# Kernel optimization log

Measured on AMD Instinct MI355X. Metric: run time of the kernel, lower is better.

The kernel has to match this reference:

```python
import jax, jax.numpy as jnp
import numpy as np

EPS = 1e-5

def _bn(x, gamma, beta, mean, var):
    # channel axis = 1; inference-style batchnorm with given stats
    shape = (1, -1) + (1,) * (x.ndim - 2)
    inv = gamma / jnp.sqrt(var + EPS)
    return x * inv.reshape(shape) + (beta - mean * inv).reshape(shape)

def _gather(f, idx):
    # f: (C, N), idx: (N, ns) -> (C, N, ns)
    return f[:, idx]

def setup_inputs() -> dict:
    key = jax.random.key(0)
    ks = jax.random.split(key, 24)
    B, N, C, NS, O = 4, 32768, 64, 16, 128
    inp = {}
    inp['xyz'] = jax.random.normal(ks[0], (B, N, 3), jnp.float32)
    inp['feature'] = jax.random.normal(ks[1], (B, C, N), jnp.float32)
    inp['idx'] = jax.random.randint(ks[2], (B, N, NS), 0, N, jnp.int64 if jax.config.jax_enable_x64 else jnp.int32)
    inp['W1'] = jax.random.normal(ks[3], (64, 3), jnp.float32)
    inp['b1'] = jax.random.normal(ks[4], (64,), jnp.float32)
    inp['g1'] = jax.random.uniform(ks[5], (64,), jnp.float32)
    inp['be1'] = jax.random.normal(ks[6], (64,), jnp.float32)
    inp['m1'] = jnp.zeros((64,), jnp.float32)
    inp['v1'] = jnp.ones((64,), jnp.float32)
    inp['W2'] = jax.random.normal(ks[7], (64, 64), jnp.float32)
    inp['b2'] = jax.random.normal(ks[8], (64,), jnp.float32)
    inp['g2'] = jax.random.uniform(ks[9], (64,), jnp.float32)
    inp['be2'] = jax.random.normal(ks[10], (64,), jnp.float32)
    inp['m2'] = jnp.zeros((64,), jnp.float32)
    inp['v2'] = jnp.ones((64,), jnp.float32)
    inp['W3'] = jax.random.normal(ks[11], (64, 64), jnp.float32)
    inp['b3'] = jax.random.normal(ks[12], (64,), jnp.float32)
    inp['Wf'] = jax.random.normal(ks[13], (O, C * 64), jnp.float32)
    inp['bf'] = jax.random.normal(ks[14], (O,), jnp.float32)
    inp['gf'] = jax.random.uniform(ks[15], (O,), jnp.float32)
    inp['bef'] = jax.random.normal(ks[16], (O,), jnp.float32)
    inp['mf'] = jnp.zeros((O,), jnp.float32)
    inp['vf'] = jnp.ones((O,), jnp.float32)
    return inp

def reference(xyz, feature, idx, W1, b1, g1, be1, m1, v1, W2, b2, g2, be2, m2, v2, W3, b3, Wf, bf, gf, bef, mf, vf):
    B, C, N = feature.shape
    xyz_t = jnp.transpose(xyz, (0, 2, 1))  # (B, 3, N)
    # grouped relative positions: (B, 3, N, ns)
    grouped_xyz = jax.vmap(_gather)(xyz_t, idx) - xyz_t[:, :, :, None]
    # WeightNet: Conv2d 1x1 layers on channel dim
    h = jnp.einsum('oc,bcns->bons', W1, grouped_xyz) + b1[None, :, None, None]
    h = jax.nn.relu(_bn(h, g1, be1, m1, v1))
    h = jnp.einsum('oc,bcns->bons', W2, h) + b2[None, :, None, None]
    h = jax.nn.relu(_bn(h, g2, be2, m2, v2))
    weights = jnp.einsum('oc,bcns->bons', W3, h) + b3[None, :, None, None]  # (B, 64, N, ns)
    # gather features per neighbor: (B, C, N, ns)
    gfeat = jax.vmap(_gather)(feature, idx)
    # per-point matmul (B,N,C,ns) @ (B,N,ns,64) -> (B,N,C,64) -> (B,N,C*64)
    agg = jnp.einsum('bcns,bwns->bncw', gfeat, weights).reshape(B, N, C * weights.shape[1])
    # final Conv1d 1x1 + BN + ReLU, output (B, O, N)
    y = jnp.einsum('of,bnf->bon', Wf, agg) + bf[None, :, None]
    return jax.nn.relu(_bn(y, gf, bef, mf, vf))
```

## Files before the change

### kernel.cpp

```cpp
#include <hip/hip_runtime.h>
#include <cstdint>
#include <cstddef>

#define EPSV 1e-5f
constexpr int Bn  = 4;
constexpr int Nn  = 32768;
constexpr int Cn  = 64;
constexpr int NSn = 16;
constexpr int On  = 128;
constexpr int Pn  = 32;
constexpr int MAIN_BLOCKS = Bn * (Nn / Pn);

typedef __attribute__((ext_vector_type(8))) short short8;
typedef __attribute__((ext_vector_type(4))) float f32x4;

static __device__ __forceinline__ unsigned short f2bf(float f) {
  union { float f; unsigned u; } v; v.f = f;
  unsigned r = v.u + 0x7fffu + ((v.u >> 16) & 1u);
  return (unsigned short)(r >> 16);
}
static __device__ __forceinline__ unsigned pack2(unsigned short a, unsigned short b) {
  return (unsigned)a | ((unsigned)b << 16);
}

constexpr size_t WS_FEATT = 0;
constexpr size_t WS_WFP   = 16u * 1024 * 1024;
constexpr size_t WS_PF    = 17u * 1024 * 1024;
constexpr size_t WS_W2F   = WS_PF + 4096;
constexpr size_t WS_W3B   = WS_W2F + 8192;

__global__ void k_params(const float* __restrict__ W1, const float* __restrict__ b1,
                         const float* __restrict__ g1, const float* __restrict__ be1,
                         const float* __restrict__ m1, const float* __restrict__ v1,
                         const float* __restrict__ W2, const float* __restrict__ b2,
                         const float* __restrict__ g2, const float* __restrict__ be2,
                         const float* __restrict__ m2, const float* __restrict__ v2,
                         const float* __restrict__ W3, const float* __restrict__ b3,
                         const float* __restrict__ bf_, const float* __restrict__ gf,
                         const float* __restrict__ bef, const float* __restrict__ mf,
                         const float* __restrict__ vf,
                         float* __restrict__ pf, unsigned short* __restrict__ W2f,
                         unsigned short* __restrict__ W3b) {
  int t = threadIdx.x;
  if (t < 64) {
    float inv1 = g1[t] * rsqrtf(v1[t] + EPSV);
    pf[t * 4 + 0] = W1[t * 3 + 0] * inv1;
    pf[t * 4 + 1] = W1[t * 3 + 1] * inv1;
    pf[t * 4 + 2] = W1[t * 3 + 2] * inv1;
    pf[t * 4 + 3] = 0.f;
    pf[256 + t] = b1[t] * inv1 + be1[t] - m1[t] * inv1;
    float inv2 = g2[t] * rsqrtf(v2[t] + EPSV);
    pf[320 + t] = b2[t] * inv2 + be2[t] - m2[t] * inv2;
    pf[384 + t] = b3[t];
    for (int k = 0; k < 64; ++k) {
      W2f[t * 64 + k] = f2bf(W2[t * 64 + k] * inv2);
      W3b[t * 64 + k] = f2bf(W3[t * 64 + k]);
    }
  }
  if (t < 128) {
    float invf = gf[t] * rsqrtf(vf[t] + EPSV);
    pf[448 + t] = bf_[t] * invf + bef[t] - mf[t] * invf;
  }
}

__global__ void k_featT(const float* __restrict__ feat, unsigned short* __restrict__ featT) {
  int blk = blockIdx.x;
  int b = blk >> 9;
  int n0 = (blk & 511) << 6;
  __shared__ float tile[64][65];
  int t = threadIdx.x;
  int n_in = t & 63;
  int c4 = t >> 6;
  const float* fb = feat + (size_t)b * Cn * Nn;
#pragma unroll
  for (int k = 0; k < 16; ++k) {
    int c = c4 * 16 + k;
    tile[c][n_in] = fb[(size_t)c * Nn + n0 + n_in];
  }
  __syncthreads();
  unsigned short* outp = featT + ((size_t)b * Nn + n0) * Cn;
  int cc = t & 63;
#pragma unroll
  for (int k = 0; k < 16; ++k) {
    int nn = c4 * 16 + k;
    outp[(size_t)nn * Cn + cc] = f2bf(tile[cc][nn]);
  }
}

__global__ void k_wfp(const float* __restrict__ Wf, const float* __restrict__ gf,
                      const float* __restrict__ vf, unsigned short* __restrict__ WfP) {
  int e = blockIdx.x * 256 + threadIdx.x;
  int rec = e >> 9, wi_ = e & 511;
  int l = wi_ >> 3, j = wi_ & 7;
  int q = rec >> 6, ks = (rec >> 3) & 7, ot = rec & 7;
  int o = ot * 16 + (l & 15);
  int kk = ks * 32 + (l >> 4) * 8 + j;
  int c = (q >> 2) * 16 + (kk >> 4);
  int w = (q & 3) * 16 + (kk & 15);
  float invf = gf[o] * rsqrtf(vf[o] + EPSV);
  WfP[e] = f2bf(Wf[(size_t)o * 4096 + c * 64 + w] * invf);
}

constexpr int SMEM_MAIN = 141312;

__launch_bounds__(512, 1)
__global__ void k_main(const float* __restrict__ xyz, const int* __restrict__ idx,
                       const unsigned short* __restrict__ featT,
                       const unsigned short* __restrict__ WfP,
                       const float* __restrict__ pf,
                       const unsigned short* __restrict__ W2f,
                       const unsigned short* __restrict__ W3b,
                       float* __restrict__ outp) {
  extern __shared__ __align__(16) char smem[];
  unsigned short* wbuf   = (unsigned short*)(smem);
  unsigned short* h1     = (unsigned short*)(smem + 65536);
  unsigned short* gbuf   = (unsigned short*)(smem + 65536);
  unsigned short* h2     = (unsigned short*)(smem + 98304);
  unsigned short* aggbuf = (unsigned short*)(smem + 98304);
  float4* gxbuf = (float4*)(smem + 131072);
  int*    idxbuf = (int*)(smem + 139264);

  const int t = threadIdx.x;
  const int lane = t & 63;
  const int wv = t >> 6;
  const int lq = lane >> 4;
  const int lm = lane & 15;
  const int blk = blockIdx.x;
  const int bb = blk >> 10;
  const int n0 = (blk & 1023) * Pn;

  const float* W1f = pf;
  const float* b1f = pf + 256;
  const float* b2f = pf + 320;
  const float* b3f = pf + 384;
  const float* bff = pf + 448;

  const short8 z8 = {0, 0, 0, 0, 0, 0, 0, 0};
  const f32x4  z4 = {0.f, 0.f, 0.f, 0.f};

  if (t < 256) {
    const float* xb = xyz + (size_t)bb * Nn * 3;
#pragma unroll
    for (int a = 0; a < 2; ++a) {
      int col = t + a * 256;
      int p_ = col >> 4, s_ = col & 15;
      int iv = idx[((size_t)bb * Nn + n0 + p_) * NSn + s_];
      idxbuf[col] = iv;
      float cx = xb[(size_t)(n0 + p_) * 3 + 0];
      float cy = xb[(size_t)(n0 + p_) * 3 + 1];
      float cz = xb[(size_t)(n0 + p_) * 3 + 2];
      gxbuf[col] = make_float4(xb[(size_t)iv * 3 + 0] - cx,
                               xb[(size_t)iv * 3 + 1] - cy,
                               xb[(size_t)iv * 3 + 2] - cz, 0.f);
    }
  }
  __syncthreads();

  for (int h = 0; h < 2; ++h) {
    if (wv < 4) {
#pragma unroll
      for (int a = 0; a < 8; ++a) {
        int aid = t + a * 256;
        int col = aid & 255;
        int oct = aid >> 8;
        float4 g = gxbuf[h * 256 + col];
        unsigned short vals[8];
#pragma unroll
        for (int jj = 0; jj < 8; ++jj) {
          int ch = oct * 8 + jj;
          float v = W1f[ch * 4 + 0] * g.x + W1f[ch * 4 + 1] * g.y +
                    W1f[ch * 4 + 2] * g.z + b1f[ch];
          vals[jj] = f2bf(fmaxf(v, 0.f));
        }
        int u = oct ^ (col & 7);
        uint4 wv4;
        wv4.x = pack2(vals[0], vals[1]); wv4.y = pack2(vals[2], vals[3]);
        wv4.z = pack2(vals[4], vals[5]); wv4.w = pack2(vals[6], vals[7]);
        *(uint4*)(h1 + (size_t)col * 64 + u * 8) = wv4;
      }
    }
    __syncthreads();

    if (wv < 4) {
      f32x4 acc2[4][4];
#pragma unroll
      for (int mt = 0; mt < 4; ++mt)
#pragma unroll
        for (int nt = 0; nt < 4; ++nt) acc2[mt][nt] = z4;
      short8 afr[4][2];
#pragma unroll
      for (int mt = 0; mt < 4; ++mt)
#pragma unroll
        for (int ks = 0; ks < 2; ++ks)
          afr[mt][ks] = *(const short8*)(W2f + (mt * 16 + lm) * 64 + ks * 32 + lq * 8);
#pragma unroll
      for (int nt = 0; nt < 4; ++nt) {
        int col = wv * 64 + nt * 16 + lm;
#pragma unroll
        for (int ks = 0; ks < 2; ++ks) {
          int u = (ks * 4 + lq) ^ (col & 7);
          short8 bfr = *(short8*)(h1 + (size_t)col * 64 + u * 8);
#pragma unroll
          for (int mt = 0; mt < 4; ++mt)
            acc2[mt][nt] = __builtin_amdgcn_mfma_f32_16x16x32_bf16(afr[mt][ks], bfr, acc2[mt][nt], 0, 0, 0);
        }
      }
#pragma unroll
      for (int mt = 0; mt < 4; ++mt)
#pragma unroll
        for (int nt = 0; nt < 4; ++nt) {
          int col = wv * 64 + nt * 16 + lm;
#pragma unroll
          for (int r = 0; r < 4; ++r) {
            int ch = mt * 16 + lq * 4 + r;
            float v = fmaxf(acc2[mt][nt][r] + b2f[ch], 0.f);
            int u = (ch >> 3) ^ (col & 7);
            h2[(size_t)col * 64 + u * 8 + (ch & 7)] = f2bf(v);
          }
        }
    }
    __syncthreads();

    if (wv < 4) {
      f32x4 acc3[4][4];
#pragma unroll
      for (int mt = 0; mt < 4; ++mt)
#pragma unroll
        for (int nt = 0; nt < 4; ++nt) acc3[mt][nt] = z4;
      short8 afr[4][2];
#pragma unroll
      for (int mt = 0; mt < 4; ++mt)
#pragma unroll
        for (int ks = 0; ks < 2; ++ks)
          afr[mt][ks] = *(const short8*)(W3b + (mt * 16 + lm) * 64 + ks * 32 + lq * 8);
#pragma unroll
      for (int nt = 0; nt < 4; ++nt) {
        int col = wv * 64 + nt * 16 + lm;
#pragma unroll
        for (int ks = 0; ks < 2; ++ks) {
          int u = (ks * 4 + lq) ^ (col & 7);
          short8 bfr = *(short8*)(h2 + (size_t)col * 64 + u * 8);
#pragma unroll
          for (int mt = 0; mt < 4; ++mt)
            acc3[mt][nt] = __builtin_amdgcn_mfma_f32_16x16x32_bf16(afr[mt][ks], bfr, acc3[mt][nt], 0, 0, 0);
        }
      }
#pragma unroll
      for (int nt = 0; nt < 4; ++nt) {
        int pl = wv * 4 + nt;
        int p_ = h * 16 + pl;
        int s_ = lm;
#pragma unroll
        for (int mt = 0; mt < 4; ++mt)
#pragma unroll
          for (int r = 0; r < 4; ++r) {
            int w_ = mt * 16 + lq * 4 + r;
            float v = acc3[mt][nt][r] + b3f[w_];
            wbuf[(size_t)p_ * 1024 + (s_ >> 3) * 512 + w_ * 8 + (s_ & 7)] = f2bf(v);
          }
      }
    }
    __syncthreads();
  }

  f32x4 accY[2] = {z4, z4};

  for (int ci = 0; ci < 4; ++ci) {
    {
      int sl = t;
      int p_ = sl >> 4, s_ = sl & 15;
      int iv = idxbuf[sl];
      const unsigned short* src = featT + ((size_t)bb * Nn + iv) * 64 + ci * 16;
      uint4 d0 = *(const uint4*)(src);
      uint4 d1 = *(const uint4*)(src + 8);
      unsigned uu[8] = {d0.x, d0.y, d0.z, d0.w, d1.x, d1.y, d1.z, d1.w};
      size_t base = (size_t)p_ * 256 + (s_ >> 3) * 128 + (s_ & 7);
#pragma unroll
      for (int k = 0; k < 8; ++k) {
        gbuf[base + (2 * k) * 8]     = (unsigned short)(uu[k] & 0xffffu);
        gbuf[base + (2 * k + 1) * 8] = (unsigned short)(uu[k] >> 16);
      }
    }
    __syncthreads();

    for (int wi = 0; wi < 4; ++wi) {
      int q = ci * 4 + wi;
      int buf = q & 1;
#pragma unroll
      for (int pp = 0; pp < 4; ++pp) {
        int p_ = wv * 4 + pp;
        short8 afr = z8, bfr = z8;
        if (lq < 2) {
          afr = *(short8*)(wbuf + (size_t)p_ * 1024 + lq * 512 + (wi * 16 + lm) * 8);
          bfr = *(short8*)(gbuf + (size_t)p_ * 256 + lq * 128 + lm * 8);
        }
        f32x4 d = __builtin_amdgcn_mfma_f32_16x16x32_bf16(afr, bfr, z4, 0, 0, 0);
        int kkb = lm * 16 + lq * 4;
        int us = (kkb >> 3) ^ (p_ & 7);
        uint2 w2v;
        w2v.x = pack2(f2bf(d[0]), f2bf(d[1]));
        w2v.y = pack2(f2bf(d[2]), f2bf(d[3]));
        *(uint2*)(aggbuf + (size_t)buf * 8192 + (size_t)p_ * 256 + us * 8 + (kkb & 7)) = w2v;
      }
      __syncthreads();
#pragma unroll
      for (int ks = 0; ks < 8; ++ks) {
        short8 wfr = *(const short8*)(WfP + ((size_t)((q * 8 + ks) * 8 + wv)) * 512 + lane * 8);
#pragma unroll
        for (int mt = 0; mt < 2; ++mt) {
          int p16 = mt * 16 + lm;
          int u = (ks * 4 + lq) ^ (p16 & 7);
          short8 afr = *(const short8*)(aggbuf + (size_t)buf * 8192 + (size_t)p16 * 256 + u * 8);
          accY[mt] = __builtin_amdgcn_mfma_f32_16x16x32_bf16(afr, wfr, accY[mt], 0, 0, 0);
        }
      }
    }
  }

  {
    int o = wv * 16 + lm;
    float bo = bff[o];
#pragma unroll
    for (int mt = 0; mt < 2; ++mt) {
      f32x4 vv;
#pragma unroll
      for (int r = 0; r < 4; ++r) vv[r] = fmaxf(accY[mt][r] + bo, 0.f);
      int p_ = mt * 16 + lq * 4;
      float* dst = outp + ((size_t)bb * On + o) * Nn + n0 + p_;
      *(f32x4*)dst = vv;
    }
  }
}

extern "C" void kernel_launch(void* const* d_in, const int* in_sizes, int n_in,
                              void* d_out, int out_size, void* d_ws, size_t ws_size,
                              hipStream_t stream) {
  const float* xyz  = (const float*)d_in[0];
  const float* feat = (const float*)d_in[1];
  const int*   idx  = (const int*)d_in[2];
  const float* W1 = (const float*)d_in[3];
  const float* b1 = (const float*)d_in[4];
  const float* g1 = (const float*)d_in[5];
  const float* be1 = (const float*)d_in[6];
  const float* m1 = (const float*)d_in[7];
  const float* v1 = (const float*)d_in[8];
  const float* W2 = (const float*)d_in[9];
  const float* b2 = (const float*)d_in[10];
  const float* g2 = (const float*)d_in[11];
  const float* be2 = (const float*)d_in[12];
  const float* m2 = (const float*)d_in[13];
  const float* v2 = (const float*)d_in[14];
  const float* W3 = (const float*)d_in[15];
  const float* b3 = (const float*)d_in[16];
  const float* Wf = (const float*)d_in[17];
  const float* bf_ = (const float*)d_in[18];
  const float* gf = (const float*)d_in[19];
  const float* bef = (const float*)d_in[20];
  const float* mf = (const float*)d_in[21];
  const float* vf = (const float*)d_in[22];

  char* ws = (char*)d_ws;
  unsigned short* featT = (unsigned short*)(ws + WS_FEATT);
  unsigned short* WfP   = (unsigned short*)(ws + WS_WFP);
  float*          pf    = (float*)(ws + WS_PF);
  unsigned short* W2f   = (unsigned short*)(ws + WS_W2F);
  unsigned short* W3b   = (unsigned short*)(ws + WS_W3B);
  float* outp = (float*)d_out;

  hipLaunchKernelGGL(k_params, dim3(1), dim3(256), 0, stream,
                     W1, b1, g1, be1, m1, v1, W2, b2, g2, be2, m2, v2,
                     W3, b3, bf_, gf, bef, mf, vf, pf, W2f, W3b);
  hipLaunchKernelGGL(k_featT, dim3(Bn * (Nn / 64)), dim3(256), 0, stream, feat, featT);
  hipLaunchKernelGGL(k_wfp, dim3(2048), dim3(256), 0, stream, Wf, gf, vf, WfP);

  hipFuncSetAttribute(reinterpret_cast<const void*>(k_main),
                      hipFuncAttributeMaxDynamicSharedMemorySize, SMEM_MAIN);
  hipLaunchKernelGGL(k_main, dim3(MAIN_BLOCKS), dim3(512), SMEM_MAIN, stream,
                     xyz, idx, featT, WfP, pf, W2f, W3b, outp);
}
```

Baseline: 680.2 us.

## Hoist per-point weight fragments into registers and pad LDS layouts

The WeightNet output is now written to LDS with packed 8-byte stores in a padded layout (row stride 72) instead of scattered 2-byte stores, and the bias b3 is loaded as float4 vectors. All per-point A fragments for the aggregation MFMA are then gathered once into registers (af[4][4]) before the channel loop rather than reloaded from LDS on every ci iteration. The gathered-feature B fragments are also hoisted out of the wi loop, and the gbuf row stride is padded to 264 to cut bank conflicts. This trades extra LDS space and registers (64 extra VGPRs for af) for fewer LDS reads and stores, with risk of register pressure at 512 threads per block.

```diff
diff --git a/kernel.cpp b/kernel.cpp
--- a/kernel.cpp
+++ b/kernel.cpp
@@ -101,7 +101,7 @@
   WfP[e] = f2bf(Wf[(size_t)o * 4096 + c * 64 + w] * invf);
 }
 
-constexpr int SMEM_MAIN = 141312;
+constexpr int SMEM_MAIN = 149504;
 
 __launch_bounds__(512, 1)
 __global__ void k_main(const float* __restrict__ xyz, const int* __restrict__ idx,
@@ -113,12 +113,12 @@
                        float* __restrict__ outp) {
   extern __shared__ __align__(16) char smem[];
   unsigned short* wbuf   = (unsigned short*)(smem);
-  unsigned short* h1     = (unsigned short*)(smem + 65536);
-  unsigned short* gbuf   = (unsigned short*)(smem + 65536);
-  unsigned short* h2     = (unsigned short*)(smem + 98304);
-  unsigned short* aggbuf = (unsigned short*)(smem + 98304);
-  float4* gxbuf = (float4*)(smem + 131072);
-  int*    idxbuf = (int*)(smem + 139264);
+  unsigned short* h1     = (unsigned short*)(smem + 73728);
+  unsigned short* gbuf   = (unsigned short*)(smem + 73728);
+  unsigned short* h2     = (unsigned short*)(smem + 106496);
+  unsigned short* aggbuf = (unsigned short*)(smem + 106496);
+  float4* gxbuf = (float4*)(smem + 139264);
+  int*    idxbuf = (int*)(smem + 147456);
 
   const int t = threadIdx.x;
   const int lane = t & 63;
@@ -132,7 +132,6 @@
   const float* W1f = pf;
   const float* b1f = pf + 256;
   const float* b2f = pf + 320;
-  const float* b3f = pf + 384;
   const float* bff = pf + 448;
 
   const short8 z8 = {0, 0, 0, 0, 0, 0, 0, 0};
@@ -228,11 +227,14 @@
 #pragma unroll
         for (int nt = 0; nt < 4; ++nt) acc3[mt][nt] = z4;
       short8 afr[4][2];
-#pragma unroll
-      for (int mt = 0; mt < 4; ++mt)
+      float4 b3v[4];
+#pragma unroll
+      for (int mt = 0; mt < 4; ++mt) {
 #pragma unroll
         for (int ks = 0; ks < 2; ++ks)
           afr[mt][ks] = *(const short8*)(W3b + (mt * 16 + lm) * 64 + ks * 32 + lq * 8);
+        b3v[mt] = *(const float4*)(pf + 384 + mt * 16 + lq * 4);
+      }
 #pragma unroll
       for (int nt = 0; nt < 4; ++nt) {
         int col = wv * 64 + nt * 16 + lm;
@@ -249,19 +251,34 @@
       for (int nt = 0; nt < 4; ++nt) {
         int pl = wv * 4 + nt;
         int p_ = h * 16 + pl;
-        int s_ = lm;
-#pragma unroll
-        for (int mt = 0; mt < 4; ++mt)
-#pragma unroll
-          for (int r = 0; r < 4; ++r) {
-            int w_ = mt * 16 + lq * 4 + r;
-            float v = acc3[mt][nt][r] + b3f[w_];
-            wbuf[(size_t)p_ * 1024 + (s_ >> 3) * 512 + w_ * 8 + (s_ & 7)] = f2bf(v);
-          }
+#pragma unroll
+        for (int mt = 0; mt < 4; ++mt) {
+          float v0 = acc3[mt][nt][0] + b3v[mt].x;
+          float v1 = acc3[mt][nt][1] + b3v[mt].y;
+          float v2 = acc3[mt][nt][2] + b3v[mt].z;
+          float v3 = acc3[mt][nt][3] + b3v[mt].w;
+          uint2 w2v;
+          w2v.x = pack2(f2bf(v0), f2bf(v1));
+          w2v.y = pack2(f2bf(v2), f2bf(v3));
+          *(uint2*)(wbuf + (size_t)p_ * 1152 + lm * 72 + mt * 16 + lq * 4) = w2v;
+        }
       }
     }
     __syncthreads();
   }
+
+  short8 af[4][4];
+#pragma unroll
+  for (int wi = 0; wi < 4; ++wi)
+#pragma unroll
+    for (int pp = 0; pp < 4; ++pp) {
+      int p_ = wv * 4 + pp;
+      union { unsigned short u[8]; short8 s; } tmp;
+#pragma unroll
+      for (int j = 0; j < 8; ++j)
+        tmp.u[j] = wbuf[(size_t)p_ * 1152 + ((lq & 1) * 8 + j) * 72 + wi * 16 + lm];
+      af[wi][pp] = (lq < 2) ? tmp.s : z8;
+    }
 
   f32x4 accY[2] = {z4, z4};
 
@@ -274,7 +291,7 @@
       uint4 d0 = *(const uint4*)(src);
       uint4 d1 = *(const uint4*)(src + 8);
       unsigned uu[8] = {d0.x, d0.y, d0.z, d0.w, d1.x, d1.y, d1.z, d1.w};
-      size_t base = (size_t)p_ * 256 + (s_ >> 3) * 128 + (s_ & 7);
+      size_t base = (size_t)p_ * 264 + (s_ >> 3) * 128 + (s_ & 7);
 #pragma unroll
       for (int k = 0; k < 8; ++k) {
         gbuf[base + (2 * k) * 8]     = (unsigned short)(uu[k] & 0xffffu);
@@ -283,18 +300,22 @@
     }
     __syncthreads();
 
+    short8 bfr[4];
+#pragma unroll
+    for (int pp = 0; pp < 4; ++pp) {
+      int p_ = wv * 4 + pp;
+      short8 v = *(short8*)(gbuf + (size_t)p_ * 264 + (lq & 1) * 128 + lm * 8);
+      bfr[pp] = (lq < 2) ? v : z8;
+    }
+
+#pragma unroll
     for (int wi = 0; wi < 4; ++wi) {
       int q = ci * 4 + wi;
       int buf = q & 1;
 #pragma unroll
       for (int pp = 0; pp < 4; ++pp) {
         int p_ = wv * 4 + pp;
-        short8 afr = z8, bfr = z8;
-        if (lq < 2) {
-          afr = *(short8*)(wbuf + (size_t)p_ * 1024 + lq * 512 + (wi * 16 + lm) * 8);
-          bfr = *(short8*)(gbuf + (size_t)p_ * 256 + lq * 128 + lm * 8);
-        }
-        f32x4 d = __builtin_amdgcn_mfma_f32_16x16x32_bf16(afr, bfr, z4, 0, 0, 0);
+        f32x4 d = __builtin_amdgcn_mfma_f32_16x16x32_bf16(af[wi][pp], bfr[pp], z4, 0, 0, 0);
         int kkb = lm * 16 + lq * 4;
         int us = (kkb >> 3) ^ (p_ & 7);
         uint2 w2v;
```

Result: slower. 971.4 us (+42.8%).

## Split fused kernel into WeightNet and aggregation kernels via global weight buffer

Applied to the files above, without the earlier changes.

Splits the single large fused kernel (141KB LDS, one block per CU) into two kernels. The first computes the WeightNet outputs and writes them to a 256MB bf16 workspace buffer. The second gathers features, computes the per-point aggregation and the final projection. Each new kernel uses much less LDS and targets up to four blocks per CU for better latency hiding. In exchange it adds a large global write and reread of the intermediate weights, and it is only taken when the workspace is big enough.

```diff
diff --git a/kernel.cpp b/kernel.cpp
--- a/kernel.cpp
+++ b/kernel.cpp
@@ -28,6 +28,8 @@
 constexpr size_t WS_PF    = 17u * 1024 * 1024;
 constexpr size_t WS_W2F   = WS_PF + 4096;
 constexpr size_t WS_W3B   = WS_W2F + 8192;
+constexpr size_t WS_WG    = 18u * 1024 * 1024;
+constexpr size_t WS_NEED_SPLIT = WS_WG + (size_t)Bn * Nn * 1024 * 2;
 
 __global__ void k_params(const float* __restrict__ W1, const float* __restrict__ b1,
                          const float* __restrict__ g1, const float* __restrict__ be1,
@@ -101,6 +103,268 @@
   WfP[e] = f2bf(Wf[(size_t)o * 4096 + c * 64 + w] * invf);
 }
 
+constexpr int SMEM_WNET = 73728;
+
+__launch_bounds__(512, 4)
+__global__ void k_wnet(const float* __restrict__ xyz, const int* __restrict__ idx,
+                       const float* __restrict__ pf,
+                       const unsigned short* __restrict__ W2f,
+                       const unsigned short* __restrict__ W3b,
+                       unsigned short* __restrict__ wg) {
+  extern __shared__ __align__(16) char smem[];
+  unsigned short* h1 = (unsigned short*)(smem);
+  unsigned short* h2 = (unsigned short*)(smem + 32768);
+  float4* gxbuf = (float4*)(smem + 65536);
+
+  const int t = threadIdx.x;
+  const int lane = t & 63;
+  const int wv = t >> 6;
+  const int lq = lane >> 4;
+  const int lm = lane & 15;
+  const int blk = blockIdx.x;
+  const int bb = blk >> 10;
+  const int n0 = (blk & 1023) * Pn;
+
+  const float* W1f = pf;
+  const float* b1f = pf + 256;
+  const float* b2f = pf + 320;
+  const float* b3f = pf + 384;
+  const f32x4 z4 = {0.f, 0.f, 0.f, 0.f};
+
+  if (t < 256) {
+    const float* xb = xyz + (size_t)bb * Nn * 3;
+#pragma unroll
+    for (int a = 0; a < 2; ++a) {
+      int col = t + a * 256;
+      int p_ = col >> 4, s_ = col & 15;
+      int iv = idx[((size_t)bb * Nn + n0 + p_) * NSn + s_];
+      float cx = xb[(size_t)(n0 + p_) * 3 + 0];
+      float cy = xb[(size_t)(n0 + p_) * 3 + 1];
+      float cz = xb[(size_t)(n0 + p_) * 3 + 2];
+      gxbuf[col] = make_float4(xb[(size_t)iv * 3 + 0] - cx,
+                               xb[(size_t)iv * 3 + 1] - cy,
+                               xb[(size_t)iv * 3 + 2] - cz, 0.f);
+    }
+  }
+  __syncthreads();
+
+  for (int h = 0; h < 2; ++h) {
+    if (wv < 4) {
+#pragma unroll
+      for (int a = 0; a < 8; ++a) {
+        int aid = t + a * 256;
+        int col = aid & 255;
+        int oct = aid >> 8;
+        float4 g = gxbuf[h * 256 + col];
+        unsigned short vals[8];
+#pragma unroll
+        for (int jj = 0; jj < 8; ++jj) {
+          int ch = oct * 8 + jj;
+          float v = W1f[ch * 4 + 0] * g.x + W1f[ch * 4 + 1] * g.y +
+                    W1f[ch * 4 + 2] * g.z + b1f[ch];
+          vals[jj] = f2bf(fmaxf(v, 0.f));
+        }
+        int u = oct ^ (col & 7);
+        uint4 wv4;
+        wv4.x = pack2(vals[0], vals[1]); wv4.y = pack2(vals[2], vals[3]);
+        wv4.z = pack2(vals[4], vals[5]); wv4.w = pack2(vals[6], vals[7]);
+        *(uint4*)(h1 + (size_t)col * 64 + u * 8) = wv4;
+      }
+    }
+    __syncthreads();
+
+    if (wv < 4) {
+      f32x4 acc2[4][4];
+#pragma unroll
+      for (int mt = 0; mt < 4; ++mt)
+#pragma unroll
+        for (int nt = 0; nt < 4; ++nt) acc2[mt][nt] = z4;
+      short8 afr[4][2];
+#pragma unroll
+      for (int mt = 0; mt < 4; ++mt)
+#pragma unroll
+        for (int ks = 0; ks < 2; ++ks)
+          afr[mt][ks] = *(const short8*)(W2f + (mt * 16 + lm) * 64 + ks * 32 + lq * 8);
+#pragma unroll
+      for (int nt = 0; nt < 4; ++nt) {
+        int col = wv * 64 + nt * 16 + lm;
+#pragma unroll
+        for (int ks = 0; ks < 2; ++ks) {
+          int u = (ks * 4 + lq) ^ (col & 7);
+          short8 bfr = *(short8*)(h1 + (size_t)col * 64 + u * 8);
+#pragma unroll
+          for (int mt = 0; mt < 4; ++mt)
+            acc2[mt][nt] = __builtin_amdgcn_mfma_f32_16x16x32_bf16(afr[mt][ks], bfr, acc2[mt][nt], 0, 0, 0);
+        }
+      }
+#pragma unroll
+      for (int mt = 0; mt < 4; ++mt)
+#pragma unroll
+        for (int nt = 0; nt < 4; ++nt) {
+          int col = wv * 64 + nt * 16 + lm;
+#pragma unroll
+          for (int r = 0; r < 4; ++r) {
+            int ch = mt * 16 + lq * 4 + r;
+            float v = fmaxf(acc2[mt][nt][r] + b2f[ch], 0.f);
+            int u = (ch >> 3) ^ (col & 7);
+            h2[(size_t)col * 64 + u * 8 + (ch & 7)] = f2bf(v);
+          }
+        }
+    }
+    __syncthreads();
+
+    if (wv < 4) {
+      f32x4 acc3[4][4];
+#pragma unroll
+      for (int mt = 0; mt < 4; ++mt)
+#pragma unroll
+        for (int nt = 0; nt < 4; ++nt) acc3[mt][nt] = z4;
+      short8 afr[4][2];
+#pragma unroll
+      for (int mt = 0; mt < 4; ++mt)
+#pragma unroll
+        for (int ks = 0; ks < 2; ++ks)
+          afr[mt][ks] = *(const short8*)(W3b + (mt * 16 + lm) * 64 + ks * 32 + lq * 8);
+#pragma unroll
+      for (int nt = 0; nt < 4; ++nt) {
+        int col = wv * 64 + nt * 16 + lm;
+#pragma unroll
+        for (int ks = 0; ks < 2; ++ks) {
+          int u = (ks * 4 + lq) ^ (col & 7);
+          short8 bfr = *(short8*)(h2 + (size_t)col * 64 + u * 8);
+#pragma unroll
+          for (int mt = 0; mt < 4; ++mt)
+            acc3[mt][nt] = __builtin_amdgcn_mfma_f32_16x16x32_bf16(afr[mt][ks], bfr, acc3[mt][nt], 0, 0, 0);
+        }
+      }
+#pragma unroll
+      for (int nt = 0; nt < 4; ++nt) {
+        int pl = wv * 4 + nt;
+        int p_ = h * 16 + pl;
+        int s_ = lm;
+        size_t pg = (size_t)((size_t)bb * Nn + n0 + p_) * 1024;
+#pragma unroll
+        for (int mt = 0; mt < 4; ++mt)
+#pragma unroll
+          for (int r = 0; r < 4; ++r) {
+            int w_ = mt * 16 + lq * 4 + r;
+            float v = acc3[mt][nt][r] + b3f[w_];
+            wg[pg + (s_ >> 3) * 512 + w_ * 8 + (s_ & 7)] = f2bf(v);
+          }
+      }
+    }
+    __syncthreads();
+  }
+}
+
+constexpr int SMEM_FINAL = 49664;
+
+__launch_bounds__(512, 4)
+__global__ void k_final(const int* __restrict__ idx,
+                        const unsigned short* __restrict__ featT,
+                        const unsigned short* __restrict__ WfP,
+                        const float* __restrict__ pf,
+                        const unsigned short* __restrict__ wg,
+                        float* __restrict__ outp) {
+  extern __shared__ __align__(16) char smem[];
+  unsigned short* gbuf   = (unsigned short*)(smem);
+  unsigned short* aggbuf = (unsigned short*)(smem + 16896);
+
+  const int t = threadIdx.x;
+  const int lane = t & 63;
+  const int wv = t >> 6;
+  const int lq = lane >> 4;
+  const int lm = lane & 15;
+  const int blk = blockIdx.x;
+  const int bb = blk >> 10;
+  const int n0 = (blk & 1023) * Pn;
+
+  const short8 z8 = {0, 0, 0, 0, 0, 0, 0, 0};
+  const f32x4  z4 = {0.f, 0.f, 0.f, 0.f};
+
+  const int p0 = t >> 4, s0 = t & 15;
+  const int iv = idx[((size_t)bb * Nn + n0 + p0) * NSn + s0];
+  const unsigned short* fsrc = featT + ((size_t)bb * Nn + iv) * 64;
+  const unsigned short* afbase = wg + ((size_t)((size_t)bb * Nn + n0 + wv * 4) * 1024)
+                                    + (lq & 1) * 512 + lm * 8;
+
+  f32x4 accY[2] = {z4, z4};
+
+  for (int ci = 0; ci < 4; ++ci) {
+    {
+      uint4 d0 = *(const uint4*)(fsrc + ci * 16);
+      uint4 d1 = *(const uint4*)(fsrc + ci * 16 + 8);
+      unsigned uu[8] = {d0.x, d0.y, d0.z, d0.w, d1.x, d1.y, d1.z, d1.w};
+      size_t base = (size_t)p0 * 264 + (s0 >> 3) * 128 + (s0 & 7);
+#pragma unroll
+      for (int k = 0; k < 8; ++k) {
+        gbuf[base + (2 * k) * 8]     = (unsigned short)(uu[k] & 0xffffu);
+        gbuf[base + (2 * k + 1) * 8] = (unsigned short)(uu[k] >> 16);
+      }
+    }
+    __syncthreads();
+
+    short8 bfr[4];
+#pragma unroll
+    for (int pp = 0; pp < 4; ++pp) {
+      int p_ = wv * 4 + pp;
+      short8 v = *(short8*)(gbuf + (size_t)p_ * 264 + (lq & 1) * 128 + lm * 8);
+      bfr[pp] = (lq < 2) ? v : z8;
+    }
+
+#pragma unroll
+    for (int wi = 0; wi < 4; ++wi) {
+      int q = ci * 4 + wi;
+      int buf = q & 1;
+      short8 wf[8];
+#pragma unroll
+      for (int ks = 0; ks < 4; ++ks)
+        wf[ks] = *(const short8*)(WfP + ((size_t)((q * 8 + ks) * 8 + wv)) * 512 + lane * 8);
+#pragma unroll
+      for (int pp = 0; pp < 4; ++pp) {
+        int p_ = wv * 4 + pp;
+        short8 afv = *(const short8*)(afbase + (size_t)pp * 1024 + wi * 128);
+        short8 afr = (lq < 2) ? afv : z8;
+        f32x4 d = __builtin_amdgcn_mfma_f32_16x16x32_bf16(afr, bfr[pp], z4, 0, 0, 0);
+        int kkb = lm * 16 + lq * 4;
+        int us = (kkb >> 3) ^ (p_ & 7);
+        uint2 w2v;
+        w2v.x = pack2(f2bf(d[0]), f2bf(d[1]));
+        w2v.y = pack2(f2bf(d[2]), f2bf(d[3]));
+        *(uint2*)(aggbuf + (size_t)buf * 8192 + (size_t)p_ * 256 + us * 8 + (kkb & 7)) = w2v;
+      }
+      __syncthreads();
+#pragma unroll
+      for (int ks = 4; ks < 8; ++ks)
+        wf[ks] = *(const short8*)(WfP + ((size_t)((q * 8 + ks) * 8 + wv)) * 512 + lane * 8);
+#pragma unroll
+      for (int ks = 0; ks < 8; ++ks) {
+#pragma unroll
+        for (int mt = 0; mt < 2; ++mt) {
+          int p16 = mt * 16 + lm;
+          int u = (ks * 4 + lq) ^ (p16 & 7);
+          short8 afr = *(const short8*)(aggbuf + (size_t)buf * 8192 + (size_t)p16 * 256 + u * 8);
+          accY[mt] = __builtin_amdgcn_mfma_f32_16x16x32_bf16(afr, wf[ks], accY[mt], 0, 0, 0);
+        }
+      }
+    }
+  }
+
+  {
+    int o = wv * 16 + lm;
+    float bo = pf[448 + o];
+#pragma unroll
+    for (int mt = 0; mt < 2; ++mt) {
+      f32x4 vv;
+#pragma unroll
+      for (int r = 0; r < 4; ++r) vv[r] = fmaxf(accY[mt][r] + bo, 0.f);
+      int p_ = mt * 16 + lq * 4;
+      float* dst = outp + ((size_t)bb * On + o) * Nn + n0 + p_;
+      *(f32x4*)dst = vv;
+    }
+  }
+}
+
 constexpr int SMEM_MAIN = 141312;
 
 __launch_bounds__(512, 1)
@@ -365,6 +629,7 @@
   float*          pf    = (float*)(ws + WS_PF);
   unsigned short* W2f   = (unsigned short*)(ws + WS_W2F);
   unsigned short* W3b   = (unsigned short*)(ws + WS_W3B);
+  unsigned short* wg    = (unsigned short*)(ws + WS_WG);
   float* outp = (float*)d_out;
 
   hipLaunchKernelGGL(k_params, dim3(1), dim3(256), 0, stream,
@@ -373,8 +638,19 @@
   hipLaunchKernelGGL(k_featT, dim3(Bn * (Nn / 64)), dim3(256), 0, stream, feat, featT);
   hipLaunchKernelGGL(k_wfp, dim3(2048), dim3(256), 0, stream, Wf, gf, vf, WfP);
 
-  hipFuncSetAttribute(reinterpret_cast<const void*>(k_main),
-                      hipFuncAttributeMaxDynamicSharedMemorySize, SMEM_MAIN);
-  hipLaunchKernelGGL(k_main, dim3(MAIN_BLOCKS), dim3(512), SMEM_MAIN, stream,
-                     xyz, idx, featT, WfP, pf, W2f, W3b, outp);
-}
+  if (ws_size >= WS_NEED_SPLIT) {
+    hipFuncSetAttribute(reinterpret_cast<const void*>(k_wnet),
+                        hipFuncAttributeMaxDynamicSharedMemorySize, SMEM_WNET);
+    hipFuncSetAttribute(reinterpret_cast<const void*>(k_final),
+                        hipFuncAttributeMaxDynamicSharedMemorySize, SMEM_FINAL);
+    hipLaunchKernelGGL(k_wnet, dim3(MAIN_BLOCKS), dim3(512), SMEM_WNET, stream,
+                       xyz, idx, pf, W2f, W3b, wg);
+    hipLaunchKernelGGL(k_final, dim3(MAIN_BLOCKS), dim3(512), SMEM_FINAL, stream,
+                       idx, featT, WfP, pf, wg, outp);
+  } else {
+    hipFuncSetAttribute(reinterpret_cast<const void*>(k_main),
+                        hipFuncAttributeMaxDynamicSharedMemorySize, SMEM_MAIN);
+    hipLaunchKernelGGL(k_main, dim3(MAIN_BLOCKS), dim3(512), SMEM_MAIN, stream,
+                       xyz, idx, featT, WfP, pf, W2f, W3b, outp);
+  }
+}
```

New measurement: 680.3 us. About the same (+0.0%).
